# Optimization experiments

Hardware: AMD Instinct MI355X
Metric: run time of the kernel (lower is better)

The kernel has to match this reference:

```python
import jax, jax.numpy as jnp
import numpy as np

B, N, M, K = 2, 65536, 8192, 32
N_CY = N_CONE = N_DISK = N_ELLIP = 16
TOTAL_GIBS = N_CY + N_CONE + N_DISK + N_ELLIP
NUM_OBSERVERS = 16
KERNEL_REACH = 1.0
EPS = 1e-8


def setup_inputs() -> dict:
    key = jax.random.key(0)
    ks = jax.random.split(key, 10)
    points = jax.random.normal(ks[0], (B, N, 3), dtype=jnp.float32)
    q_coords = jax.random.normal(ks[1], (B, M, 3), dtype=jnp.float32)
    support_idxs = jax.random.randint(ks[2], (B, M, K), 0, N)
    mc_points = jax.random.normal(ks[3], (1024, 3), dtype=jnp.float32)
    # per-GIB geometric params, positive, within kernel reach (random_init analogue)
    u = lambda k, shp: 0.1 + (KERNEL_REACH - 0.1) * jax.random.uniform(k, shp, dtype=jnp.float32)
    cy_params = u(ks[4], (N_CY, 2))      # [radius, sigma]
    cone_params = u(ks[5], (N_CONE, 2))  # [slope, sigma]
    disk_params = u(ks[6], (N_DISK, 2))  # [radius, height]
    ellip_params = u(ks[7], (N_ELLIP, 3))  # [rx, ry, rz]
    # cvx coefficients: softmax over GIB axis (maintain_convexity at init)
    lambdas = jax.nn.softmax(jax.random.normal(ks[8], (TOTAL_GIBS, NUM_OBSERVERS), dtype=jnp.float32), axis=0)
    return {"points": points, "q_coords": q_coords, "support_idxs": support_idxs,
            "mc_points": mc_points, "cy_params": cy_params, "cone_params": cone_params,
            "disk_params": disk_params, "ellip_params": ellip_params, "lambdas": lambdas}


def _gib_outputs(points, q_coords, support_idxs, cy_p, cone_p, disk_p, ellip_p):
    # shared neighborhood gather: (B, M, K, 3)
    supp = points[jnp.arange(points.shape[0])[:, None, None], support_idxs]
    rel = supp - q_coords[:, :, None, :]
    rx, ry, rz = rel[..., 0], rel[..., 1], rel[..., 2]
    r2 = rx * rx + ry * ry                     # (B, M, K) squared radial dist
    r2e, rze = r2[..., None], rz[..., None]    # (B, M, K, 1)
    # cylinder: gaussian shell around radius in the xy-plane
    cy = jnp.exp(-(r2e - cy_p[:, 0] ** 2) ** 2 / (2.0 * cy_p[:, 1] ** 2 + EPS))
    # cone: radial distance tracks slope * height
    cone = jnp.exp(-(jnp.sqrt(r2e + EPS) - cone_p[:, 0] * rze) ** 2 / (2.0 * cone_p[:, 1] ** 2 + EPS))
    # disk: flattened gaussian (wide radially, thin in z)
    disk = jnp.exp(-r2e / (disk_p[:, 0] ** 2 + EPS) - rze ** 2 / (disk_p[:, 1] ** 2 + EPS))
    # ellipsoid: anisotropic gaussian
    el = jnp.exp(-(rx[..., None] ** 2 / (ellip_p[:, 0] ** 2 + EPS)
                   + ry[..., None] ** 2 / (ellip_p[:, 1] ** 2 + EPS)
                   + rz[..., None] ** 2 / (ellip_p[:, 2] ** 2 + EPS)))
    # reduce over neighborhood K, then stack GIBs: (B, M, total_gibs)
    return jnp.concatenate([cy.mean(axis=2), cone.mean(axis=2),
                            disk.mean(axis=2), el.mean(axis=2)], axis=-1)


def reference(points, q_coords, support_idxs, mc_points, cy_params, cone_params,
              disk_params, ellip_params, lambdas):
    q_out = _gib_outputs(points, q_coords, support_idxs,
                         cy_params, cone_params, disk_params, ellip_params)
    # observers: convex combination of GIB responses -> (B, M, num_observers)
    return q_out @ lambdas
```

## Files before the change

kernel.cpp:

```cpp
#include <hip/hip_runtime.h>


#define EPSF 1e-8f
#define LOG2E 1.4426950408889634f

constexpr int Mq   = 8192;
constexpr int Kc   = 32;
constexpr int QPB  = 32;
constexpr int KPT  = 4;

__global__ __launch_bounds__(256) void gib_kernel(
    const float* __restrict__ points,
    const float* __restrict__ qc,
    const int*   __restrict__ sidx,
    const float* __restrict__ cyp,
    const float* __restrict__ conep,
    const float* __restrict__ diskp,
    const float* __restrict__ ellp,
    const float* __restrict__ lam,
    float*       __restrict__ out)
{
    __shared__ float pk[16][12];
    __shared__ float lamS[64 * 16];

    const int tid = threadIdx.x;

    if (tid < 16) {
        float c0 = cyp[2 * tid], c1 = cyp[2 * tid + 1];
        pk[tid][0] = c0 * c0;
        pk[tid][1] = LOG2E / (2.f * c1 * c1 + EPSF);
        float k0 = conep[2 * tid], k1 = conep[2 * tid + 1];
        pk[tid][2] = k0;
        pk[tid][3] = LOG2E / (2.f * k1 * k1 + EPSF);
        float d0 = diskp[2 * tid], d1 = diskp[2 * tid + 1];
        pk[tid][4] = LOG2E / (d0 * d0 + EPSF);
        pk[tid][5] = LOG2E / (d1 * d1 + EPSF);
        float e0 = ellp[3 * tid], e1 = ellp[3 * tid + 1], e2 = ellp[3 * tid + 2];
        pk[tid][6] = LOG2E / (e0 * e0 + EPSF);
        pk[tid][7] = LOG2E / (e1 * e1 + EPSF);
        pk[tid][8] = LOG2E / (e2 * e2 + EPSF);
        pk[tid][9] = 0.f; pk[tid][10] = 0.f; pk[tid][11] = 0.f;
    }
#pragma unroll
    for (int i = 0; i < 4; i++)
        lamS[tid * 4 + i] = lam[tid * 4 + i] * (1.0f / 32.0f);
    __syncthreads();

    const int q   = blockIdx.x * QPB + (tid >> 3);
    const int sub = tid & 7;
    const int b   = q >> 13;

    const float* qcp = qc + q * 3;
    const float qx = qcp[0], qy = qcp[1], qz = qcp[2];

    const float* ptbase = points + (size_t)b * (65536 * 3);

    const int4 idx4 = ((const int4*)(sidx + q * Kc))[sub];
    const int idxs[KPT] = {idx4.x, idx4.y, idx4.z, idx4.w};

    float r2a[KPT], sa[KPT], rza[KPT], rx2a[KPT], ry2a[KPT], rz2a[KPT];
#pragma unroll
    for (int j = 0; j < KPT; j++) {
        const float* pp = ptbase + idxs[j] * 3;
        float rx = pp[0] - qx;
        float ry = pp[1] - qy;
        float rz = pp[2] - qz;
        float rx2 = rx * rx, ry2 = ry * ry, rz2 = rz * rz;
        float r2 = rx2 + ry2;
        r2a[j] = r2;
        sa[j]  = sqrtf(r2 + EPSF);
        rza[j] = rz;
        rx2a[j] = rx2; ry2a[j] = ry2; rz2a[j] = rz2;
    }

    float acc[64];
#pragma unroll
    for (int g = 0; g < 16; g++) {
        const float4 pA = *(const float4*)&pk[g][0];
        const float4 pB = *(const float4*)&pk[g][4];
        const float4 pC = *(const float4*)&pk[g][8];
        float scy = 0.f, sco = 0.f, sdk = 0.f, sel = 0.f;
#pragma unroll
        for (int j = 0; j < KPT; j++) {
            float t = r2a[j] - pA.x;
            scy += exp2f(-(t * t) * pA.y);
            float u = fmaf(-pA.z, rza[j], sa[j]);
            sco += exp2f(-(u * u) * pA.w);
            sdk += exp2f(-fmaf(r2a[j], pB.x, rz2a[j] * pB.y));
            sel += exp2f(-fmaf(rx2a[j], pB.z, fmaf(ry2a[j], pB.w, rz2a[j] * pC.x)));
        }
        acc[g]      = scy;
        acc[16 + g] = sco;
        acc[32 + g] = sdk;
        acc[48 + g] = sel;
    }

#pragma unroll
    for (int m = 1; m < 8; m <<= 1) {
#pragma unroll
        for (int g = 0; g < 64; g++) acc[g] += __shfl_xor(acc[g], m, 64);
    }

    const int o = sub * 2;
    float s0 = 0.f, s1 = 0.f;
#pragma unroll
    for (int g = 0; g < 64; g++) {
        const float2 l = *(const float2*)&lamS[g * 16 + o];
        s0 = fmaf(acc[g], l.x, s0);
        s1 = fmaf(acc[g], l.y, s1);
    }

    float2 w;
    w.x = s0;
    w.y = s1;
    *(float2*)(out + q * 16 + o) = w;
}

extern "C" void kernel_launch(void* const* d_in, const int* in_sizes, int n_in,
                              void* d_out, int out_size, void* d_ws, size_t ws_size,
                              hipStream_t stream) {
    const float* points = (const float*)d_in[0];
    const float* qc     = (const float*)d_in[1];
    const int*   sidx   = (const int*)d_in[2];
    const float* cyp    = (const float*)d_in[4];
    const float* conep  = (const float*)d_in[5];
    const float* diskp  = (const float*)d_in[6];
    const float* ellp   = (const float*)d_in[7];
    const float* lam    = (const float*)d_in[8];
    float*       out    = (float*)d_out;

    const int totalQ = 2 * Mq;
    dim3 grid(totalQ / QPB), block(256);
    hipLaunchKernelGGL(gib_kernel, grid, block, 0, stream,
                       points, qc, sidx, cyp, conep, diskp, ellp, lam, out);
}
```

Measured before the change: 85.56 us.

## Restructure GIB kernel to stage neighbor geometry in LDS and map lanes to GIBs

Neighbor geometry (r2, sqrt, rz, squared components) is now computed once per (query, neighbor) and staged in shared memory. Each thread then handles one GIB index for one query and loops over all 32 neighbors, so it holds 4 accumulators instead of 64. The 64x16 lambda projection is reduced with a recursive-halving shuffle transpose across 16 lanes, replacing 64-wide butterfly shuffles. This is meant to cut register pressure and shuffle count so occupancy can rise, at the cost of extra LDS traffic and a block-wide barrier.

```diff
diff --git a/kernel.cpp b/kernel.cpp
--- a/kernel.cpp
+++ b/kernel.cpp
@@ -4,12 +4,11 @@
 #define EPSF 1e-8f
 #define LOG2E 1.4426950408889634f
 
-constexpr int Mq   = 8192;
-constexpr int Kc   = 32;
-constexpr int QPB  = 32;
-constexpr int KPT  = 4;
+constexpr int QPB         = 16;
+constexpr int GEO_QSTRIDE = 264;
+constexpr int LAM_STRIDE  = 20;
 
-__global__ __launch_bounds__(256) void gib_kernel(
+__global__ __launch_bounds__(256, 4) void gib_kernel(
     const float* __restrict__ points,
     const float* __restrict__ qc,
     const int*   __restrict__ sidx,
@@ -20,100 +19,144 @@
     const float* __restrict__ lam,
     float*       __restrict__ out)
 {
-    __shared__ float pk[16][12];
-    __shared__ float lamS[64 * 16];
+    __shared__ float  geo[QPB * GEO_QSTRIDE];
+    __shared__ float  lamS[64 * LAM_STRIDE];
+    __shared__ float4 pkA[16];
+    __shared__ float4 pkB[16];
+    __shared__ float  pkC[16];
 
     const int tid = threadIdx.x;
 
     if (tid < 16) {
         float c0 = cyp[2 * tid], c1 = cyp[2 * tid + 1];
-        pk[tid][0] = c0 * c0;
-        pk[tid][1] = LOG2E / (2.f * c1 * c1 + EPSF);
         float k0 = conep[2 * tid], k1 = conep[2 * tid + 1];
-        pk[tid][2] = k0;
-        pk[tid][3] = LOG2E / (2.f * k1 * k1 + EPSF);
         float d0 = diskp[2 * tid], d1 = diskp[2 * tid + 1];
-        pk[tid][4] = LOG2E / (d0 * d0 + EPSF);
-        pk[tid][5] = LOG2E / (d1 * d1 + EPSF);
         float e0 = ellp[3 * tid], e1 = ellp[3 * tid + 1], e2 = ellp[3 * tid + 2];
-        pk[tid][6] = LOG2E / (e0 * e0 + EPSF);
-        pk[tid][7] = LOG2E / (e1 * e1 + EPSF);
-        pk[tid][8] = LOG2E / (e2 * e2 + EPSF);
-        pk[tid][9] = 0.f; pk[tid][10] = 0.f; pk[tid][11] = 0.f;
-    }
-#pragma unroll
-    for (int i = 0; i < 4; i++)
-        lamS[tid * 4 + i] = lam[tid * 4 + i] * (1.0f / 32.0f);
-    __syncthreads();
-
-    const int q   = blockIdx.x * QPB + (tid >> 3);
-    const int sub = tid & 7;
-    const int b   = q >> 13;
-
-    const float* qcp = qc + q * 3;
-    const float qx = qcp[0], qy = qcp[1], qz = qcp[2];
-
-    const float* ptbase = points + (size_t)b * (65536 * 3);
-
-    const int4 idx4 = ((const int4*)(sidx + q * Kc))[sub];
-    const int idxs[KPT] = {idx4.x, idx4.y, idx4.z, idx4.w};
-
-    float r2a[KPT], sa[KPT], rza[KPT], rx2a[KPT], ry2a[KPT], rz2a[KPT];
-#pragma unroll
-    for (int j = 0; j < KPT; j++) {
-        const float* pp = ptbase + idxs[j] * 3;
-        float rx = pp[0] - qx;
-        float ry = pp[1] - qy;
-        float rz = pp[2] - qz;
-        float rx2 = rx * rx, ry2 = ry * ry, rz2 = rz * rz;
-        float r2 = rx2 + ry2;
-        r2a[j] = r2;
-        sa[j]  = sqrtf(r2 + EPSF);
-        rza[j] = rz;
-        rx2a[j] = rx2; ry2a[j] = ry2; rz2a[j] = rz2;
+        pkA[tid] = make_float4(c0 * c0, -LOG2E / (2.f * c1 * c1 + EPSF),
+                               k0,      -LOG2E / (2.f * k1 * k1 + EPSF));
+        pkB[tid] = make_float4(-LOG2E / (d0 * d0 + EPSF), -LOG2E / (d1 * d1 + EPSF),
+                               -LOG2E / (e0 * e0 + EPSF), -LOG2E / (e1 * e1 + EPSF));
+        pkC[tid] = -LOG2E / (e2 * e2 + EPSF);
     }
 
-    float acc[64];
+    {
+        int g = tid >> 2, c = (tid & 3) * 4;
 #pragma unroll
-    for (int g = 0; g < 16; g++) {
-        const float4 pA = *(const float4*)&pk[g][0];
-        const float4 pB = *(const float4*)&pk[g][4];
-        const float4 pC = *(const float4*)&pk[g][8];
-        float scy = 0.f, sco = 0.f, sdk = 0.f, sel = 0.f;
-#pragma unroll
-        for (int j = 0; j < KPT; j++) {
-            float t = r2a[j] - pA.x;
-            scy += exp2f(-(t * t) * pA.y);
-            float u = fmaf(-pA.z, rza[j], sa[j]);
-            sco += exp2f(-(u * u) * pA.w);
-            sdk += exp2f(-fmaf(r2a[j], pB.x, rz2a[j] * pB.y));
-            sel += exp2f(-fmaf(rx2a[j], pB.z, fmaf(ry2a[j], pB.w, rz2a[j] * pC.x)));
-        }
-        acc[g]      = scy;
-        acc[16 + g] = sco;
-        acc[32 + g] = sdk;
-        acc[48 + g] = sel;
+        for (int j = 0; j < 4; j++)
+            lamS[g * LAM_STRIDE + c + j] = lam[g * 16 + c + j] * (1.0f / 32.0f);
     }
 
 #pragma unroll
-    for (int m = 1; m < 8; m <<= 1) {
-#pragma unroll
-        for (int g = 0; g < 64; g++) acc[g] += __shfl_xor(acc[g], m, 64);
+    for (int it = 0; it < 2; it++) {
+        int i  = tid + it * 256;
+        int ql = i >> 5, k = i & 31;
+        int qg = blockIdx.x * QPB + ql;
+        int b  = qg >> 13;
+        int idx = sidx[qg * 32 + k];
+        const float* pp = points + ((size_t)(b << 16) + idx) * 3;
+        const float* qq = qc + qg * 3;
+        float rx = pp[0] - qq[0];
+        float ry = pp[1] - qq[1];
+        float rz = pp[2] - qq[2];
+        float rx2 = rx * rx, ry2 = ry * ry, rz2 = rz * rz;
+        float r2 = rx2 + ry2;
+        float s  = sqrtf(r2 + EPSF);
+        float* gp = &geo[ql * GEO_QSTRIDE + k * 8];
+        *(float4*)gp       = make_float4(r2, s, rz, rx2);
+        *(float4*)(gp + 4) = make_float4(ry2, rz2, 0.f, 0.f);
+    }
+    __syncthreads();
+
+    const int l  = tid & 63;
+    const int ql = (tid >> 6) * 4 + (l >> 4);
+    const int lg = l & 15;
+
+    const float4 pA = pkA[lg];
+    const float4 pB = pkB[lg];
+    const float  eC = pkC[lg];
+
+    float a0 = 0.f, a1 = 0.f, a2 = 0.f, a3 = 0.f;
+    const float* gq = &geo[ql * GEO_QSTRIDE];
+#pragma unroll 8
+    for (int k = 0; k < 32; k++) {
+        float4 ga = *(const float4*)(gq + k * 8);
+        float2 gb = *(const float2*)(gq + k * 8 + 4);
+        float r2 = ga.x, s = ga.y, rz = ga.z, rx2 = ga.w;
+        float ry2 = gb.x, rz2 = gb.y;
+        float t = r2 - pA.x;
+        a0 += exp2f(t * t * pA.y);
+        float u = fmaf(-pA.z, rz, s);
+        a1 += exp2f(u * u * pA.w);
+        a2 += exp2f(fmaf(r2, pB.x, rz2 * pB.y));
+        a3 += exp2f(fmaf(rx2, pB.z, fmaf(ry2, pB.w, rz2 * eC)));
     }
 
-    const int o = sub * 2;
-    float s0 = 0.f, s1 = 0.f;
+    float sv[16];
 #pragma unroll
-    for (int g = 0; g < 64; g++) {
-        const float2 l = *(const float2*)&lamS[g * 16 + o];
-        s0 = fmaf(acc[g], l.x, s0);
-        s1 = fmaf(acc[g], l.y, s1);
+    for (int i = 0; i < 16; i++) sv[i] = 0.f;
+    const float accs[4] = {a0, a1, a2, a3};
+#pragma unroll
+    for (int t = 0; t < 4; t++) {
+        const float* lrow = &lamS[(t * 16 + lg) * LAM_STRIDE];
+        float4 L0 = *(const float4*)(lrow);
+        float4 L1 = *(const float4*)(lrow + 4);
+        float4 L2 = *(const float4*)(lrow + 8);
+        float4 L3 = *(const float4*)(lrow + 12);
+        float a = accs[t];
+        sv[0]  = fmaf(a, L0.x, sv[0]);
+        sv[8]  = fmaf(a, L0.y, sv[8]);
+        sv[4]  = fmaf(a, L0.z, sv[4]);
+        sv[12] = fmaf(a, L0.w, sv[12]);
+        sv[2]  = fmaf(a, L1.x, sv[2]);
+        sv[10] = fmaf(a, L1.y, sv[10]);
+        sv[6]  = fmaf(a, L1.z, sv[6]);
+        sv[14] = fmaf(a, L1.w, sv[14]);
+        sv[1]  = fmaf(a, L2.x, sv[1]);
+        sv[9]  = fmaf(a, L2.y, sv[9]);
+        sv[5]  = fmaf(a, L2.z, sv[5]);
+        sv[13] = fmaf(a, L2.w, sv[13]);
+        sv[3]  = fmaf(a, L3.x, sv[3]);
+        sv[11] = fmaf(a, L3.y, sv[11]);
+        sv[7]  = fmaf(a, L3.z, sv[7]);
+        sv[15] = fmaf(a, L3.w, sv[15]);
     }
 
-    float2 w;
-    w.x = s0;
-    w.y = s1;
-    *(float2*)(out + q * 16 + o) = w;
+    {
+        bool up = (lg & 1);
+#pragma unroll
+        for (int i = 0; i < 8; i++) {
+            float keep = up ? sv[i + 8] : sv[i];
+            float send = up ? sv[i] : sv[i + 8];
+            sv[i] = keep + __shfl_xor(send, 1, 64);
+        }
+    }
+    {
+        bool up = (lg & 2);
+#pragma unroll
+        for (int i = 0; i < 4; i++) {
+            float keep = up ? sv[i + 4] : sv[i];
+            float send = up ? sv[i] : sv[i + 4];
+            sv[i] = keep + __shfl_xor(send, 2, 64);
+        }
+    }
+    {
+        bool up = (lg & 4);
+#pragma unroll
+        for (int i = 0; i < 2; i++) {
+            float keep = up ? sv[i + 2] : sv[i];
+            float send = up ? sv[i] : sv[i + 2];
+            sv[i] = keep + __shfl_xor(send, 4, 64);
+        }
+    }
+    {
+        bool up = (lg & 8);
+        float keep = up ? sv[1] : sv[0];
+        float send = up ? sv[0] : sv[1];
+        sv[0] = keep + __shfl_xor(send, 8, 64);
+    }
+
+    const int qg = blockIdx.x * QPB + ql;
+    out[qg * 16 + lg] = sv[0];
 }
 
 extern "C" void kernel_launch(void* const* d_in, const int* in_sizes, int n_in,
@@ -129,7 +172,7 @@
     const float* lam    = (const float*)d_in[8];
     float*       out    = (float*)d_out;
 
-    const int totalQ = 2 * Mq;
+    const int totalQ = 2 * 8192;
     dim3 grid(totalQ / QPB), block(256);
     hipLaunchKernelGGL(gib_kernel, grid, block, 0, stream,
                        points, qc, sidx, cyp, conep, diskp, ellp, lam, out);
```

Result: no change. 87.02 us (+1.7%).
